# Kernel optimization log

Measured on AMD Instinct MI355X. Metric: run time of the kernel, lower is better.

Reference implementation:

```python
import jax, jax.numpy as jnp
import numpy as np

B, T, D = 64, 256, 1024
H, HS = 16, 64
FF = 4096
EPS = 1e-5


def _layernorm(x, g, b):
    mu = jnp.mean(x, axis=-1, keepdims=True)
    var = jnp.mean(jnp.square(x - mu), axis=-1, keepdims=True)
    return (x - mu) * jax.lax.rsqrt(var + EPS) * g + b


def setup_inputs() -> dict:
    key = jax.random.key(0)
    ks = jax.random.split(key, 12)
    s = 0.02
    return {
        "x": jax.random.normal(ks[0], (B, T, D), jnp.float32),
        "ln1_g": jnp.ones((D,), jnp.float32),
        "ln1_b": jnp.zeros((D,), jnp.float32),
        "Wq": jax.random.normal(ks[1], (H, D, HS), jnp.float32) * s,
        "Wk": jax.random.normal(ks[2], (H, D, HS), jnp.float32) * s,
        "Wv": jax.random.normal(ks[3], (H, D, HS), jnp.float32) * s,
        "Wproj": jax.random.normal(ks[4], (D, D), jnp.float32) * s,
        "bproj": jnp.zeros((D,), jnp.float32),
        "ln2_g": jnp.ones((D,), jnp.float32),
        "ln2_b": jnp.zeros((D,), jnp.float32),
        "W1": jax.random.normal(ks[5], (D, FF), jnp.float32) * s,
        "b1": jnp.zeros((FF,), jnp.float32),
        "W2": jax.random.normal(ks[6], (FF, D), jnp.float32) * s,
        "b2": jnp.zeros((D,), jnp.float32),
    }


def reference(x, ln1_g, ln1_b, Wq, Wk, Wv, Wproj, bproj, ln2_g, ln2_b, W1, b1, W2, b2):
    # x = ln1(x)
    h = _layernorm(x, ln1_g, ln1_b)
    # per-head Q/K/V projections, batched over heads
    q = jnp.einsum("btd,hde->bhte", h, Wq)
    k = jnp.einsum("btd,hde->bhte", h, Wk)
    v = jnp.einsum("btd,hde->bhte", h, Wv)
    # NOTE: source scales by C**-0.5 with C = input_size (D), not head_size
    scale = D ** -0.5
    scores = jnp.einsum("bhte,bhse->bhts", q, k) * scale
    causal = jnp.tril(jnp.ones((T, T), bool))
    scores = jnp.where(causal, scores, -jnp.inf)
    w = jax.nn.softmax(scores, axis=-1)  # dropout is identity in eval
    attn = jnp.einsum("bhts,bhse->bthe", w, v).reshape(x.shape[0], x.shape[1], H * HS)
    sa = attn @ Wproj + bproj
    # residual onto ln1 output (as written in source)
    y = h + sa
    h2 = _layernorm(y, ln2_g, ln2_b)
    ff = jax.nn.relu(h2 @ W1 + b1) @ W2 + b2
    return h2 + ff
```

## Files before the change

### kernel.cpp

```cpp
#include <hip/hip_runtime.h>

typedef __bf16 bf16x8 __attribute__((ext_vector_type(8)));
typedef float f32x4 __attribute__((ext_vector_type(4)));
typedef unsigned short ushort_t;

__device__ __forceinline__ ushort_t f2bf(float f) {
  unsigned int u = __float_as_uint(f);
  u += 0x7fffu + ((u >> 16) & 1u);
  return (ushort_t)(u >> 16);
}

__device__ __forceinline__ void gl_lds16(const ushort_t* g, const char* l) {
  __builtin_amdgcn_global_load_lds(
      (const __attribute__((address_space(1))) void*)g,
      (__attribute__((address_space(3))) void*)l, 16, 0, 0);
}

__global__ __launch_bounds__(256) void fill_k(float* __restrict__ p, long n, float v) {
  long i = (long)blockIdx.x * 256 + threadIdx.x;
  if (i < n) p[i] = v;
}

__global__ __launch_bounds__(256) void transpose_w(const float* __restrict__ in,
                                                   ushort_t* __restrict__ out,
                                                   int R, int C) {
  __shared__ float tile[32][33];
  const float* inb = in + (long)blockIdx.z * R * C;
  ushort_t* outb = out + (long)blockIdx.z * R * C;
  int r0 = blockIdx.x * 32, c0 = blockIdx.y * 32;
  int tx = threadIdx.x & 31, ty = threadIdx.x >> 5;
#pragma unroll
  for (int i = ty; i < 32; i += 8) tile[i][tx] = inb[(long)(r0 + i) * C + (c0 + tx)];
  __syncthreads();
#pragma unroll
  for (int i = ty; i < 32; i += 8) outb[(long)(c0 + i) * R + (r0 + tx)] = f2bf(tile[tx][i]);
}

__global__ __launch_bounds__(256) void ln_k(const float* __restrict__ x,
                                            const float* __restrict__ g,
                                            const float* __restrict__ b,
                                            float* __restrict__ outF,
                                            ushort_t* __restrict__ outU) {
  __shared__ float red[8];
  long row = blockIdx.x;
  int tid = threadIdx.x;
  float4 v = ((const float4*)(x + row * 1024))[tid];
  float s = v.x + v.y + v.z + v.w;
#pragma unroll
  for (int off = 32; off; off >>= 1) s += __shfl_xor(s, off);
  int w = tid >> 6;
  if ((tid & 63) == 0) red[w] = s;
  __syncthreads();
  float mean = (red[0] + red[1] + red[2] + red[3]) * (1.0f / 1024.0f);
  float dx = v.x - mean, dy = v.y - mean, dz = v.z - mean, dw = v.w - mean;
  float s2 = dx * dx + dy * dy + dz * dz + dw * dw;
#pragma unroll
  for (int off = 32; off; off >>= 1) s2 += __shfl_xor(s2, off);
  if ((tid & 63) == 0) red[4 + w] = s2;
  __syncthreads();
  float var = (red[4] + red[5] + red[6] + red[7]) * (1.0f / 1024.0f);
  float rstd = rsqrtf(var + 1e-5f);
  int c = tid * 4;
  float o0 = dx * rstd * g[c + 0] + b[c + 0];
  float o1 = dy * rstd * g[c + 1] + b[c + 1];
  float o2 = dz * rstd * g[c + 2] + b[c + 2];
  float o3 = dw * rstd * g[c + 3] + b[c + 3];
  ((float4*)(outF + row * 1024))[tid] = make_float4(o0, o1, o2, o3);
  ushort4 u;
  u.x = f2bf(o0); u.y = f2bf(o1); u.z = f2bf(o2); u.w = f2bf(o3);
  ((ushort4*)(outU + row * 1024))[tid] = u;
}

template <int EPI>
__global__ __launch_bounds__(512, 2) void gemm256(const ushort_t* __restrict__ A,
                                                  const ushort_t* __restrict__ Bt,
                                                  int M, int N, int K, int NBC,
                                                  const float* __restrict__ bias,
                                                  const float* res, float* outF,
                                                  ushort_t* __restrict__ outU,
                                                  ushort_t* __restrict__ outU2,
                                                  ushort_t* __restrict__ outU3) {
  __shared__ __align__(16) char lds[131072];
  const int tid = threadIdx.x;
  const int lane = tid & 63;
  const int w = tid >> 6;
  const int wr = w >> 2, wc = w & 3;
  const int g = lane >> 4, lr = lane & 15;
  const int cpx = gridDim.x >> 3;
  const int wg = (blockIdx.x & 7) * cpx + (blockIdx.x >> 3);
  const long m0 = (long)(wg / NBC) * 256;
  const long n0 = (long)(wg % NBC) * 256;
  const int srow = tid >> 3;
  const int sslot = (tid & 7) ^ (srow & 7);
  const ushort_t* sA = A + (m0 + srow) * (long)K + sslot * 8;
  const ushort_t* sB = Bt + (n0 + srow) * (long)K + sslot * 8;
  const int dA = tid * 16;
  const int dB = 32768 + tid * 16;
  const int abase = (wr * 128 + lr) * 128;
  const int bbase = 32768 + (wc * 64 + lr) * 128;
  const int s0 = g ^ (lr & 7);
  const int s1 = (4 + g) ^ (lr & 7);
  const int NT = K >> 6;

  f32x4 acc[8][4] = {};
  bf16x8 aR[4][2], bR[4][2];
  const char* rb;

#define STAGE_A(tile, half) do {                                          \
    const long _ko = (long)(tile) * 64;                                   \
    char* _d = lds + (((tile) & 1) << 16) + ((half) << 14) + dA;          \
    gl_lds16(sA + _ko + (long)(2 * (half)) * 64 * K, _d);                 \
    gl_lds16(sA + _ko + (long)(2 * (half) + 1) * 64 * K, _d + 8192);      \
  } while (0)
#define STAGE_B(tile, half) do {                                          \
    const long _ko = (long)(tile) * 64;                                   \
    char* _d = lds + (((tile) & 1) << 16) + ((half) << 14) + dB;          \
    gl_lds16(sB + _ko + (long)(2 * (half)) * 64 * K, _d);                 \
    gl_lds16(sB + _ko + (long)(2 * (half) + 1) * 64 * K, _d + 8192);      \
  } while (0)
#define RD_A(base_mf) do {                                                \
    _Pragma("unroll") for (int mf = 0; mf < 4; ++mf) {                    \
      aR[mf][0] = *(const bf16x8*)(rb + abase + ((base_mf) + mf) * 2048 + s0 * 16); \
      aR[mf][1] = *(const bf16x8*)(rb + abase + ((base_mf) + mf) * 2048 + s1 * 16); \
    } } while (0)
#define RD_B2(base_nf) do {                                               \
    _Pragma("unroll") for (int nf = 0; nf < 2; ++nf) {                    \
      bR[(base_nf) + nf][0] = *(const bf16x8*)(rb + bbase + ((base_nf) + nf) * 2048 + s0 * 16); \
      bR[(base_nf) + nf][1] = *(const bf16x8*)(rb + bbase + ((base_nf) + nf) * 2048 + s1 * 16); \
    } } while (0)
#define QUAD(MB, NB) do {                                                 \
    __builtin_amdgcn_s_setprio(1);                                        \
    _Pragma("unroll") for (int mf = 0; mf < 4; ++mf)                      \
      _Pragma("unroll") for (int nf = 0; nf < 2; ++nf) {                  \
        acc[(MB) + mf][(NB) + nf] = __builtin_amdgcn_mfma_f32_16x16x32_bf16(aR[mf][0], bR[(NB) + nf][0], acc[(MB) + mf][(NB) + nf], 0, 0, 0); \
        acc[(MB) + mf][(NB) + nf] = __builtin_amdgcn_mfma_f32_16x16x32_bf16(aR[mf][1], bR[(NB) + nf][1], acc[(MB) + mf][(NB) + nf], 0, 0, 0); \
      }                                                                   \
    __builtin_amdgcn_s_setprio(0); } while (0)
#define LGKM0 do {                                                        \
    asm volatile("s_waitcnt lgkmcnt(0)" ::: "memory");                    \
    __builtin_amdgcn_sched_barrier(0); } while (0)

  STAGE_B(0, 0); STAGE_B(0, 1); STAGE_A(0, 0); STAGE_A(0, 1);
  STAGE_B(1, 0); STAGE_B(1, 1); STAGE_A(1, 0);
  asm volatile("s_waitcnt vmcnt(6)" ::: "memory");
  __builtin_amdgcn_s_barrier();

  for (int t = 0; t < NT; t += 2) {
    const bool s2 = (t + 2 < NT), s3 = (t + 3 < NT);
    rb = lds;
    RD_A(0);
    RD_B2(0);
    STAGE_A(t + 1, 1);
    asm volatile("s_waitcnt lgkmcnt(8)" ::: "memory");
    __builtin_amdgcn_s_barrier();
    LGKM0;
    QUAD(0, 0);
    __builtin_amdgcn_s_barrier();
    RD_B2(2);
    __builtin_amdgcn_s_barrier();
    LGKM0;
    QUAD(0, 2);
    __builtin_amdgcn_s_barrier();
    if (s2) STAGE_B(t + 2, 0);
    RD_A(4);
    __builtin_amdgcn_s_barrier();
    LGKM0;
    QUAD(4, 2);
    __builtin_amdgcn_s_barrier();
    if (s2) { STAGE_B(t + 2, 1); STAGE_A(t + 2, 0); }
    __builtin_amdgcn_s_barrier();
    QUAD(4, 0);
    if (s2) asm volatile("s_waitcnt vmcnt(6)" ::: "memory");
    else    asm volatile("s_waitcnt vmcnt(0)" ::: "memory");
    __builtin_amdgcn_s_barrier();
    rb = lds + 65536;
    RD_A(0);
    RD_B2(0);
    if (s2) STAGE_A(t + 2, 1);
    asm volatile("s_waitcnt lgkmcnt(8)" ::: "memory");
    __builtin_amdgcn_s_barrier();
    LGKM0;
    QUAD(0, 0);
    __builtin_amdgcn_s_barrier();
    RD_B2(2);
    __builtin_amdgcn_s_barrier();
    LGKM0;
    QUAD(0, 2);
    __builtin_amdgcn_s_barrier();
    if (s3) STAGE_B(t + 3, 0);
    RD_A(4);
    __builtin_amdgcn_s_barrier();
    LGKM0;
    QUAD(4, 2);
    __builtin_amdgcn_s_barrier();
    if (s3) { STAGE_B(t + 3, 1); STAGE_A(t + 3, 0); }
    __builtin_amdgcn_s_barrier();
    QUAD(4, 0);
    if (s3) asm volatile("s_waitcnt vmcnt(6)" ::: "memory");
    else    asm volatile("s_waitcnt vmcnt(0)" ::: "memory");
    __builtin_amdgcn_s_barrier();
  }
#undef STAGE_A
#undef STAGE_B
#undef RD_A
#undef RD_B2
#undef QUAD
#undef LGKM0

  if constexpr (EPI == 4) {
    const int p = (int)(n0 >> 10);
    const long bb2 = m0 >> 8;
    if (p < 2) {
      ushort_t* dst = (p == 0) ? outU : outU2;
#pragma unroll
      for (int mf = 0; mf < 8; ++mf)
#pragma unroll
        for (int nf = 0; nf < 4; ++nf)
#pragma unroll
          for (int r = 0; r < 4; ++r) {
            long tt = (wr * 128 + mf * 16 + g * 4 + r);
            long cc = (n0 & 1023) + wc * 64 + nf * 16 + lr;
            long hh = cc >> 6, e = cc & 63;
            dst[(((bb2 * 16 + hh) * 256 + tt) << 6) + e] = f2bf(acc[mf][nf][r]);
          }
    } else {
      unsigned int* l32 = (unsigned int*)lds;
#pragma unroll
      for (int mf = 0; mf < 8; ++mf)
#pragma unroll
        for (int nf = 0; nf < 4; ++nf)
#pragma unroll
          for (int r2 = 0; r2 < 2; ++r2) {
            int row = wr * 128 + mf * 16 + g * 4 + r2 * 2;
            int col = wc * 64 + nf * 16 + lr;
            unsigned int pk = (unsigned int)f2bf(acc[mf][nf][r2 * 2]) |
                              ((unsigned int)f2bf(acc[mf][nf][r2 * 2 + 1]) << 16);
            l32[col * 128 + ((row >> 1) ^ ((col & 7) << 2))] = pk;
          }
      __syncthreads();
      const long vcol0 = (n0 & 1023);
#pragma unroll
      for (int k = 0; k < 16; ++k) {
        int c = tid + k * 512;
        int e_l = c >> 5, k16 = c & 31;
        uint4 d = *(uint4*)&l32[e_l * 128 + ((k16 * 4) ^ ((e_l & 7) << 2))];
        long vc = vcol0 + e_l;
        long hh = vc >> 6, e = vc & 63;
        *(uint4*)&outU3[(((bb2 * 16 + hh) * 64 + e) << 8) + k16 * 8] = d;
      }
    }
  } else {
#pragma unroll
    for (int mf = 0; mf < 8; ++mf)
#pragma unroll
      for (int nf = 0; nf < 4; ++nf)
#pragma unroll
        for (int r = 0; r < 4; ++r) {
          long row = m0 + wr * 128 + mf * 16 + g * 4 + r;
          long col = n0 + wc * 64 + nf * 16 + lr;
          float v = acc[mf][nf][r];
          if constexpr (EPI == 2) {
            long i = row * N + col;
            outF[i] = v + bias[col] + res[i];
          } else {
            outU[row * N + col] = f2bf(fmaxf(v + bias[col], 0.0f));
          }
        }
  }
}

__global__ __launch_bounds__(64) void attn_k(const ushort_t* __restrict__ q,
                                             const ushort_t* __restrict__ k,
                                             const ushort_t* __restrict__ vt,
                                             ushort_t* __restrict__ ao) {
  __shared__ __align__(16) ushort_t Ps[64][40];
  const int lane = threadIdx.x;
  const int g = lane >> 4, lr = lane & 15;
  const int blk = blockIdx.x;
  const int q4 = blk & 3;
  const int bh = blk >> 2;
  const int bb = bh >> 4, hh = bh & 15;
  const int q0 = q4 * 64;
  const ushort_t* qb = q + (long)bh * 256 * 64;
  const ushort_t* kb = k + (long)bh * 256 * 64;
  const ushort_t* vb = vt + (long)bh * 64 * 256;
  bf16x8 qf[4][2];
#pragma unroll
  for (int m = 0; m < 4; m++)
#pragma unroll
    for (int ks = 0; ks < 2; ks++)
      qf[m][ks] = *(const bf16x8*)(qb + (q0 + m * 16 + lr) * 64 + ks * 32 + g * 8);
  f32x4 o[4][4] = {};
  float mrow[4][4], lrow[4][4];
#pragma unroll
  for (int m = 0; m < 4; m++)
#pragma unroll
    for (int r = 0; r < 4; r++) { mrow[m][r] = -__builtin_inff(); lrow[m][r] = 0.0f; }
  const float scale = 0.03125f;
  const int nkb = q0 / 32 + 2;
  for (int kbk = 0; kbk < nkb; kbk++) {
    f32x4 s[4][2] = {};
#pragma unroll
    for (int ks = 0; ks < 2; ks++) {
      bf16x8 kf[2];
#pragma unroll
      for (int n = 0; n < 2; n++)
        kf[n] = *(const bf16x8*)(kb + (kbk * 32 + n * 16 + lr) * 64 + ks * 32 + g * 8);
#pragma unroll
      for (int m = 0; m < 4; m++)
#pragma unroll
        for (int n = 0; n < 2; n++)
          s[m][n] = __builtin_amdgcn_mfma_f32_16x16x32_bf16(qf[m][ks], kf[n], s[m][n], 0, 0, 0);
    }
#pragma unroll
    for (int m = 0; m < 4; m++)
#pragma unroll
      for (int n = 0; n < 2; n++)
#pragma unroll
        for (int r = 0; r < 4; r++) {
          int row = q0 + m * 16 + g * 4 + r;
          int col = kbk * 32 + n * 16 + lr;
          float v = s[m][n][r] * scale;
          s[m][n][r] = (col <= row) ? v : -1e30f;
        }
#pragma unroll
    for (int m = 0; m < 4; m++)
#pragma unroll
      for (int r = 0; r < 4; r++) {
        float mx = fmaxf(s[m][0][r], s[m][1][r]);
#pragma unroll
        for (int off = 8; off; off >>= 1) mx = fmaxf(mx, __shfl_xor(mx, off));
        float mn = fmaxf(mrow[m][r], mx);
        float alpha = __expf(mrow[m][r] - mn);
        mrow[m][r] = mn;
        float rs = 0.0f;
#pragma unroll
        for (int n = 0; n < 2; n++) {
          float p = __expf(s[m][n][r] - mn);
          s[m][n][r] = p;
          rs += p;
        }
#pragma unroll
        for (int off = 8; off; off >>= 1) rs += __shfl_xor(rs, off);
        lrow[m][r] = lrow[m][r] * alpha + rs;
#pragma unroll
        for (int n = 0; n < 4; n++) o[m][n][r] *= alpha;
      }
#pragma unroll
    for (int m = 0; m < 4; m++)
#pragma unroll
      for (int n = 0; n < 2; n++)
#pragma unroll
        for (int r = 0; r < 4; r++)
          Ps[m * 16 + g * 4 + r][n * 16 + lr] = f2bf(s[m][n][r]);
    __syncthreads();
    bf16x8 vf[4];
#pragma unroll
    for (int n = 0; n < 4; n++)
      vf[n] = *(const bf16x8*)(vb + (n * 16 + lr) * 256 + kbk * 32 + g * 8);
#pragma unroll
    for (int m = 0; m < 4; m++) {
      bf16x8 pa = *(const bf16x8*)&Ps[m * 16 + lr][g * 8];
#pragma unroll
      for (int n = 0; n < 4; n++)
        o[m][n] = __builtin_amdgcn_mfma_f32_16x16x32_bf16(pa, vf[n], o[m][n], 0, 0, 0);
    }
    __syncthreads();
  }
#pragma unroll
  for (int m = 0; m < 4; m++)
#pragma unroll
    for (int r = 0; r < 4; r++) {
      float inv = 1.0f / lrow[m][r];
      long t = q0 + m * 16 + g * 4 + r;
#pragma unroll
      for (int n = 0; n < 4; n++) {
        long e = n * 16 + lr;
        ao[((long)bb * 256 + t) * 1024 + hh * 64 + e] = f2bf(o[m][n][r] * inv);
      }
    }
}

extern "C" void kernel_launch(void* const* d_in, const int* in_sizes, int n_in,
                              void* d_out, int out_size, void* d_ws, size_t ws_size,
                              hipStream_t stream) {
  const float* x     = (const float*)d_in[0];
  const float* ln1g  = (const float*)d_in[1];
  const float* ln1b  = (const float*)d_in[2];
  const float* Wq    = (const float*)d_in[3];
  const float* Wk    = (const float*)d_in[4];
  const float* Wv    = (const float*)d_in[5];
  const float* Wproj = (const float*)d_in[6];
  const float* bproj = (const float*)d_in[7];
  const float* ln2g  = (const float*)d_in[8];
  const float* ln2b  = (const float*)d_in[9];
  const float* W1    = (const float*)d_in[10];
  const float* b1    = (const float*)d_in[11];
  const float* W2    = (const float*)d_in[12];
  const float* b2    = (const float*)d_in[13];

  const long NEED = 184L << 20;
  if (ws_size < (size_t)NEED) {
    fill_k<<<(out_size + 255) / 256, 256, 0, stream>>>((float*)d_out, out_size,
                                                       (float)(ws_size >> 20));
    return;
  }

  char* ws = (char*)d_ws;
  const long MB = 1 << 20;
  ushort_t* wqt = (ushort_t*)(ws + 0 * MB);
  ushort_t* wkt = (ushort_t*)(ws + 2 * MB);
  ushort_t* wvt = (ushort_t*)(ws + 4 * MB);
  ushort_t* wpt = (ushort_t*)(ws + 6 * MB);
  ushort_t* w1t = (ushort_t*)(ws + 8 * MB);
  ushort_t* w2t = (ushort_t*)(ws + 16 * MB);
  ushort_t* hb  = (ushort_t*)(ws + 24 * MB);
  ushort_t* qbf = (ushort_t*)(ws + 56 * MB);
  ushort_t* kbf = (ushort_t*)(ws + 88 * MB);
  ushort_t* vtb = (ushort_t*)(ws + 120 * MB);
  ushort_t* atb = (ushort_t*)(ws + 152 * MB);
  ushort_t* ff1 = (ushort_t*)(ws + 56 * MB);
  float*    yf  = (float*)d_out;

  transpose_w<<<dim3(32, 2, 16), 256, 0, stream>>>(Wq, wqt, 1024, 64);
  transpose_w<<<dim3(32, 2, 16), 256, 0, stream>>>(Wk, wkt, 1024, 64);
  transpose_w<<<dim3(32, 2, 16), 256, 0, stream>>>(Wv, wvt, 1024, 64);
  transpose_w<<<dim3(32, 32, 1), 256, 0, stream>>>(Wproj, wpt, 1024, 1024);
  transpose_w<<<dim3(32, 128, 1), 256, 0, stream>>>(W1, w1t, 1024, 4096);
  transpose_w<<<dim3(128, 32, 1), 256, 0, stream>>>(W2, w2t, 4096, 1024);

  ln_k<<<16384, 256, 0, stream>>>(x, ln1g, ln1b, yf, hb);
  gemm256<4><<<768, 512, 0, stream>>>(hb, wqt, 16384, 3072, 1024, 12,
                                      nullptr, nullptr, nullptr, qbf, kbf, vtb);
  attn_k<<<4096, 64, 0, stream>>>(qbf, kbf, vtb, atb);
  gemm256<2><<<256, 512, 0, stream>>>(atb, wpt, 16384, 1024, 1024, 4,
                                      bproj, yf, yf, nullptr, nullptr, nullptr);
  ln_k<<<16384, 256, 0, stream>>>(yf, ln2g, ln2b, yf, hb);
  gemm256<3><<<1024, 512, 0, stream>>>(hb, w1t, 16384, 4096, 1024, 16,
                                       b1, nullptr, nullptr, ff1, nullptr, nullptr);
  gemm256<2><<<256, 512, 0, stream>>>(ff1, w2t, 16384, 1024, 4096, 4,
                                      b2, yf, yf, nullptr, nullptr, nullptr);
}
```

Baseline: 635.2 us.

## Shrink attention query tile, mask only diagonal block, use lazy rescale

The attention kernel now processes 32 query rows per block instead of 64, doubling the grid and cutting wasted fully-masked key blocks. It applies the causal mask only on the diagonal key block, folds log2(e) into the scale so it can use exp2f, and skips the running-max rescale unless the max grows by more than a threshold. It also hoists the V loads earlier and drops the __syncthreads, which is valid only because the block is a single wavefront. The lazy rescale trades exactness of the max tracking for fewer multiplies, and the smaller tile lowers reuse of the K and V loads.

New measurement: 638.0 us. Within noise of the previous version (+0.4%).

```diff
diff --git a/kernel.cpp b/kernel.cpp
--- a/kernel.cpp
+++ b/kernel.cpp
@@ -269,37 +269,37 @@
   }
 }
 
-__global__ __launch_bounds__(64) void attn_k(const ushort_t* __restrict__ q,
-                                             const ushort_t* __restrict__ k,
-                                             const ushort_t* __restrict__ vt,
-                                             ushort_t* __restrict__ ao) {
-  __shared__ __align__(16) ushort_t Ps[64][40];
+__global__ __launch_bounds__(64, 4) void attn_k(const ushort_t* __restrict__ q,
+                                                const ushort_t* __restrict__ k,
+                                                const ushort_t* __restrict__ vt,
+                                                ushort_t* __restrict__ ao) {
+  __shared__ __align__(16) ushort_t Ps[32][40];
   const int lane = threadIdx.x;
   const int g = lane >> 4, lr = lane & 15;
   const int blk = blockIdx.x;
-  const int q4 = blk & 3;
-  const int bh = blk >> 2;
+  const int q8 = blk & 7;
+  const int bh = blk >> 3;
   const int bb = bh >> 4, hh = bh & 15;
-  const int q0 = q4 * 64;
+  const int q0 = q8 * 32;
   const ushort_t* qb = q + (long)bh * 256 * 64;
   const ushort_t* kb = k + (long)bh * 256 * 64;
   const ushort_t* vb = vt + (long)bh * 64 * 256;
-  bf16x8 qf[4][2];
-#pragma unroll
-  for (int m = 0; m < 4; m++)
+  bf16x8 qf[2][2];
+#pragma unroll
+  for (int m = 0; m < 2; m++)
 #pragma unroll
     for (int ks = 0; ks < 2; ks++)
       qf[m][ks] = *(const bf16x8*)(qb + (q0 + m * 16 + lr) * 64 + ks * 32 + g * 8);
-  f32x4 o[4][4] = {};
-  float mrow[4][4], lrow[4][4];
-#pragma unroll
-  for (int m = 0; m < 4; m++)
-#pragma unroll
-    for (int r = 0; r < 4; r++) { mrow[m][r] = -__builtin_inff(); lrow[m][r] = 0.0f; }
-  const float scale = 0.03125f;
-  const int nkb = q0 / 32 + 2;
+  f32x4 o[2][4] = {};
+  float mrow[2][4], lrow[2][4];
+#pragma unroll
+  for (int m = 0; m < 2; m++)
+#pragma unroll
+    for (int r = 0; r < 4; r++) { mrow[m][r] = -3.0e38f; lrow[m][r] = 0.0f; }
+  const float sc2 = 0.04508422f;
+  const int nkb = q8 + 1;
   for (int kbk = 0; kbk < nkb; kbk++) {
-    f32x4 s[4][2] = {};
+    f32x4 s[2][2] = {};
 #pragma unroll
     for (int ks = 0; ks < 2; ks++) {
       bf16x8 kf[2];
@@ -307,68 +307,91 @@
       for (int n = 0; n < 2; n++)
         kf[n] = *(const bf16x8*)(kb + (kbk * 32 + n * 16 + lr) * 64 + ks * 32 + g * 8);
 #pragma unroll
-      for (int m = 0; m < 4; m++)
+      for (int m = 0; m < 2; m++)
 #pragma unroll
         for (int n = 0; n < 2; n++)
           s[m][n] = __builtin_amdgcn_mfma_f32_16x16x32_bf16(qf[m][ks], kf[n], s[m][n], 0, 0, 0);
     }
-#pragma unroll
-    for (int m = 0; m < 4; m++)
-#pragma unroll
-      for (int n = 0; n < 2; n++)
+    bf16x8 vf[4];
+#pragma unroll
+    for (int n = 0; n < 4; n++)
+      vf[n] = *(const bf16x8*)(vb + (n * 16 + lr) * 256 + kbk * 32 + g * 8);
+    if (kbk == q8) {
+#pragma unroll
+      for (int m = 0; m < 2; m++)
+#pragma unroll
+        for (int n = 0; n < 2; n++)
+#pragma unroll
+          for (int r = 0; r < 4; r++) {
+            int row = q0 + m * 16 + g * 4 + r;
+            int col = kbk * 32 + n * 16 + lr;
+            s[m][n][r] = (col <= row) ? s[m][n][r] * sc2 : -3.0e38f;
+          }
+    } else {
+#pragma unroll
+      for (int m = 0; m < 2; m++)
+#pragma unroll
+        for (int n = 0; n < 2; n++)
+#pragma unroll
+          for (int r = 0; r < 4; r++) s[m][n][r] *= sc2;
+    }
+    float mx[2][4];
+    float growth = -3.0e38f;
+#pragma unroll
+    for (int m = 0; m < 2; m++)
+#pragma unroll
+      for (int r = 0; r < 4; r++) {
+        float v = fmaxf(s[m][0][r], s[m][1][r]);
+#pragma unroll
+        for (int off = 8; off; off >>= 1) v = fmaxf(v, __shfl_xor(v, off));
+        mx[m][r] = v;
+        growth = fmaxf(growth, v - mrow[m][r]);
+      }
+    if (__any(growth > 8.0f)) {
+#pragma unroll
+      for (int m = 0; m < 2; m++)
 #pragma unroll
         for (int r = 0; r < 4; r++) {
-          int row = q0 + m * 16 + g * 4 + r;
-          int col = kbk * 32 + n * 16 + lr;
-          float v = s[m][n][r] * scale;
-          s[m][n][r] = (col <= row) ? v : -1e30f;
+          float mn = fmaxf(mrow[m][r], mx[m][r]);
+          float al = exp2f(mrow[m][r] - mn);
+          mrow[m][r] = mn;
+          lrow[m][r] *= al;
+#pragma unroll
+          for (int n = 0; n < 4; n++) o[m][n][r] *= al;
         }
-#pragma unroll
-    for (int m = 0; m < 4; m++)
+    }
+#pragma unroll
+    for (int m = 0; m < 2; m++)
 #pragma unroll
       for (int r = 0; r < 4; r++) {
-        float mx = fmaxf(s[m][0][r], s[m][1][r]);
-#pragma unroll
-        for (int off = 8; off; off >>= 1) mx = fmaxf(mx, __shfl_xor(mx, off));
-        float mn = fmaxf(mrow[m][r], mx);
-        float alpha = __expf(mrow[m][r] - mn);
-        mrow[m][r] = mn;
         float rs = 0.0f;
 #pragma unroll
         for (int n = 0; n < 2; n++) {
-          float p = __expf(s[m][n][r] - mn);
+          float p = exp2f(s[m][n][r] - mrow[m][r]);
           s[m][n][r] = p;
           rs += p;
         }
 #pragma unroll
         for (int off = 8; off; off >>= 1) rs += __shfl_xor(rs, off);
-        lrow[m][r] = lrow[m][r] * alpha + rs;
-#pragma unroll
-        for (int n = 0; n < 4; n++) o[m][n][r] *= alpha;
+        lrow[m][r] += rs;
       }
 #pragma unroll
-    for (int m = 0; m < 4; m++)
+    for (int m = 0; m < 2; m++)
 #pragma unroll
       for (int n = 0; n < 2; n++)
 #pragma unroll
         for (int r = 0; r < 4; r++)
           Ps[m * 16 + g * 4 + r][n * 16 + lr] = f2bf(s[m][n][r]);
-    __syncthreads();
-    bf16x8 vf[4];
-#pragma unroll
-    for (int n = 0; n < 4; n++)
-      vf[n] = *(const bf16x8*)(vb + (n * 16 + lr) * 256 + kbk * 32 + g * 8);
-#pragma unroll
-    for (int m = 0; m < 4; m++) {
+#pragma unroll
+    for (int m = 0; m < 2; m++) {
       bf16x8 pa = *(const bf16x8*)&Ps[m * 16 + lr][g * 8];
 #pragma unroll
       for (int n = 0; n < 4; n++)
         o[m][n] = __builtin_amdgcn_mfma_f32_16x16x32_bf16(pa, vf[n], o[m][n], 0, 0, 0);
     }
-    __syncthreads();
   }
 #pragma unroll
-  for (int m = 0; m < 4; m++)
+  for (int m = 0; m < 2; m++)
 #pragma unroll
     for (int r = 0; r < 4; r++) {
       float inv = 1.0f / lrow[m][r];
@@ -432,7 +455,7 @@
   ln_k<<<16384, 256, 0, stream>>>(x, ln1g, ln1b, yf, hb);
   gemm256<4><<<768, 512, 0, stream>>>(hb, wqt, 16384, 3072, 1024, 12,
                                       nullptr, nullptr, nullptr, qbf, kbf, vtb);
-  attn_k<<<4096, 64, 0, stream>>>(qbf, kbf, vtb, atb);
+  attn_k<<<8192, 64, 0, stream>>>(qbf, kbf, vtb, atb);
   gemm256<2><<<256, 512, 0, stream>>>(atb, wpt, 16384, 1024, 1024, 4,
                                       bproj, yf, yf, nullptr, nullptr, nullptr);
   ln_k<<<16384, 256, 0, stream>>>(yf, ln2g, ln2b, yf, hb);
```
